# Kernel tuning notes

Measured on AMD Instinct MI355X. Metric: run time of the kernel, lower is better.

Reference implementation:

```python
import jax, jax.numpy as jnp
import numpy as np

N_NODES = 50000
N_EDGES = 800000
IN_CH = 128
HID = 128
N_GRAPHS = 512


def setup_inputs() -> dict:
    key = jax.random.key(0)
    ks = jax.random.split(key, 12)
    x = jax.random.normal(ks[0], (N_NODES, IN_CH), dtype=jnp.float32)
    edge_index = jax.random.randint(ks[1], (2, N_EDGES), 0, N_NODES, dtype=jnp.int64)
    batch = jnp.sort(jax.random.randint(ks[2], (N_NODES,), 0, N_GRAPHS, dtype=jnp.int64))
    s = 0.05
    params = {
        'W1l': jax.random.normal(ks[3], (HID, IN_CH), dtype=jnp.float32) * s,
        'W1r': jax.random.normal(ks[4], (HID, IN_CH), dtype=jnp.float32) * s,
        'b1': jax.random.normal(ks[5], (HID,), dtype=jnp.float32) * s,
        'W2l': jax.random.normal(ks[6], (HID, HID), dtype=jnp.float32) * s,
        'W2r': jax.random.normal(ks[7], (HID, HID), dtype=jnp.float32) * s,
        'b2': jax.random.normal(ks[8], (HID,), dtype=jnp.float32) * s,
        'W3l': jax.random.normal(ks[9], (HID, HID), dtype=jnp.float32) * s,
        'W3r': jax.random.normal(ks[10], (HID, HID), dtype=jnp.float32) * s,
        'b3': jax.random.normal(ks[11], (HID,), dtype=jnp.float32) * s,
    }
    return {'x': x, 'edge_index': edge_index, 'batch': batch, **params}


def reference(x, edge_index, batch, W1l, W1r, b1, W2l, W2r, b2, W3l, W3r, b3):
    src = edge_index[0]
    dst = edge_index[1]
    n = x.shape[0]
    # in-degree for mean aggregation (nodes with no in-edges get 0 aggregate)
    deg = jax.ops.segment_sum(jnp.ones((src.shape[0],), x.dtype), dst, num_segments=n)
    inv_deg = (1.0 / jnp.maximum(deg, 1.0))[:, None]  # [N,1]

    def sage(h, Wl, Wr, b):
        # gather neighbor feats, scatter-mean to targets, then linear + root term
        agg = jax.ops.segment_sum(h[src], dst, num_segments=n) * inv_deg  # [N,d]
        return agg @ Wl.T + h @ Wr.T + b

    h = jax.nn.relu(sage(x, W1l, W1r, b1))
    h = jax.nn.relu(sage(h, W2l, W2r, b2))
    h = jax.nn.relu(sage(h, W3l, W3r, b3))

    # global mean pool over graph ids
    counts = jax.ops.segment_sum(jnp.ones((n,), h.dtype), batch, num_segments=N_GRAPHS)
    pooled = jax.ops.segment_sum(h, batch, num_segments=N_GRAPHS)
    return pooled / jnp.maximum(counts, 1.0)[:, None]
```

## Files before the change

### kernel.cpp

```cpp
#include <hip/hip_runtime.h>

#define N_NODES 50000
#define NP 50048
#define N_EDGES 800000
#define N_GRAPHS 512
#define F 128
#define ELLW 64

#define FILL_BLOCKS 3125
#define CASTX_BLOCKS 3128
#define CASTW_BLOCKS 48

typedef __bf16 bf16x8 __attribute__((ext_vector_type(8)));
typedef float f32x4 __attribute__((ext_vector_type(4)));
typedef unsigned short ushort_t;
typedef unsigned int uint_t;

__device__ inline ushort_t f2bf(float f) {
    uint_t u = __float_as_uint(f);
    u += 0x7FFFu + ((u >> 16) & 1u);
    return (ushort_t)(u >> 16);
}
__device__ inline float bf2f(ushort_t u) {
    return __uint_as_float(((uint_t)u) << 16);
}
__device__ inline uint_t pack2(float a, float b) {
    return (uint_t)f2bf(a) | ((uint_t)f2bf(b) << 16);
}

__global__ __launch_bounds__(256) void k_build(
    const float* __restrict__ x,
    const float* __restrict__ w0, const float* __restrict__ w1,
    const float* __restrict__ w2, const float* __restrict__ w3,
    const float* __restrict__ w4, const float* __restrict__ w5,
    const int* __restrict__ src, const int* __restrict__ dst,
    ushort_t* __restrict__ X, ushort_t* __restrict__ WB,
    int* __restrict__ cnt, ushort_t* __restrict__ ell) {
    int b = blockIdx.x;
    int t = threadIdx.x;
    if (b < FILL_BLOCKS) {
        int e = b * 256 + t;
        int d = dst[e];
        int pos = atomicAdd(&cnt[d], 1);
        if (pos < ELLW) ell[(d << 6) + pos] = (ushort_t)src[e];
    } else if (b < FILL_BLOCKS + CASTX_BLOCKS) {
        int i = ((b - FILL_BLOCKS) * 256 + t) * 8;
        uint4 o = make_uint4(0, 0, 0, 0);
        if (i < N_NODES * F) {
            float4 v0 = *(const float4*)&x[i];
            float4 v1 = *(const float4*)&x[i + 4];
            o = make_uint4(pack2(v0.x, v0.y), pack2(v0.z, v0.w),
                           pack2(v1.x, v1.y), pack2(v1.z, v1.w));
        }
        *(uint4*)&X[i] = o;
    } else {
        int idx = (b - FILL_BLOCKS - CASTX_BLOCKS) * 256 + t;
        int m = idx >> 11;
        int o = (idx & 2047) * 8;
        const float* s = w0;
        if (m == 1) s = w1; else if (m == 2) s = w2; else if (m == 3) s = w3;
        else if (m == 4) s = w4; else if (m == 5) s = w5;
        float4 v0 = *(const float4*)&s[o];
        float4 v1 = *(const float4*)&s[o + 4];
        *(uint4*)&WB[m * 16384 + o] =
            make_uint4(pack2(v0.x, v0.y), pack2(v0.z, v0.w),
                       pack2(v1.x, v1.y), pack2(v1.z, v1.w));
    }
}

__device__ inline void addrow(float* a, uint4 v) {
    a[0] += __uint_as_float(v.x << 16); a[1] += __uint_as_float(v.x & 0xFFFF0000u);
    a[2] += __uint_as_float(v.y << 16); a[3] += __uint_as_float(v.y & 0xFFFF0000u);
    a[4] += __uint_as_float(v.z << 16); a[5] += __uint_as_float(v.z & 0xFFFF0000u);
    a[6] += __uint_as_float(v.w << 16); a[7] += __uint_as_float(v.w & 0xFFFF0000u);
}

__global__ __launch_bounds__(256) void k_gather(const ushort_t* __restrict__ h,
                                                const ushort_t* __restrict__ ell,
                                                const int* __restrict__ cnt,
                                                ushort_t* __restrict__ agg) {
    int t = blockIdx.x * 256 + threadIdx.x;
    int n = t >> 4;
    int lane = t & 15;
    if (n >= N_NODES) return;
    int deg = min(cnt[n], ELLW);
    const ushort_t* el = ell + (n << 6);
    const uint4* h4 = (const uint4*)h;
    float ax[8], ay[8];
#pragma unroll
    for (int j = 0; j < 8; j++) { ax[j] = 0.f; ay[j] = 0.f; }
    int i = 0;
    for (; i + 8 <= deg; i += 8) {
        uint4 iv = *(const uint4*)&el[i];
        int s0 = iv.x & 0xFFFF, s1 = iv.x >> 16;
        int s2 = iv.y & 0xFFFF, s3 = iv.y >> 16;
        int s4 = iv.z & 0xFFFF, s5 = iv.z >> 16;
        int s6 = iv.w & 0xFFFF, s7 = iv.w >> 16;
        uint4 v0 = h4[(size_t)s0 * 16 + lane];
        uint4 v1 = h4[(size_t)s1 * 16 + lane];
        uint4 v2 = h4[(size_t)s2 * 16 + lane];
        uint4 v3 = h4[(size_t)s3 * 16 + lane];
        uint4 v4 = h4[(size_t)s4 * 16 + lane];
        uint4 v5 = h4[(size_t)s5 * 16 + lane];
        uint4 v6 = h4[(size_t)s6 * 16 + lane];
        uint4 v7 = h4[(size_t)s7 * 16 + lane];
        addrow(ax, v0); addrow(ay, v1); addrow(ax, v2); addrow(ay, v3);
        addrow(ax, v4); addrow(ay, v5); addrow(ax, v6); addrow(ay, v7);
    }
    for (; i < deg; i++) {
        uint4 v0 = h4[(size_t)el[i] * 16 + lane];
        addrow(ax, v0);
    }
    float sc = 1.0f / fmaxf((float)deg, 1.0f);
    uint_t r[4];
#pragma unroll
    for (int j = 0; j < 4; j++)
        r[j] = pack2((ax[2 * j] + ay[2 * j]) * sc,
                     (ax[2 * j + 1] + ay[2 * j + 1]) * sc);
    ((uint4*)agg)[(size_t)n * 16 + lane] = make_uint4(r[0], r[1], r[2], r[3]);
}

__global__ __launch_bounds__(256) void k_linear(const ushort_t* __restrict__ agg,
                                                const ushort_t* h,
                                                const ushort_t* __restrict__ Wl,
                                                const ushort_t* __restrict__ Wr,
                                                const float* __restrict__ bias,
                                                ushort_t* out) {
    __shared__ uint4 Alds4[512];
    __shared__ uint4 Blds4[1024];
    ushort_t* Alds = (ushort_t*)Alds4;
    ushort_t* Blds = (ushort_t*)Blds4;

    int t = threadIdx.x;
    int w = t >> 6;
    int lane = t & 63;
    int bm = blockIdx.x * 64;
    int wm = (w & 1) * 32;
    int wn = (w >> 1) * 64;
    int lrow = lane & 15;
    int kg = lane >> 4;

    f32x4 acc[2][4];
#pragma unroll
    for (int i = 0; i < 2; i++)
#pragma unroll
        for (int j = 0; j < 4; j++) acc[i][j] = (f32x4){0.f, 0.f, 0.f, 0.f};

    for (int iter = 0; iter < 4; iter++) {
        int kk = iter * 64;
        const ushort_t* A = (kk < 128) ? agg : h;
        const ushort_t* W = (kk < 128) ? Wl : Wr;
        int k0 = kk & 127;

        __syncthreads();
#pragma unroll
        for (int p = 0; p < 2; p++) {
            int chunkA = p * 4 + w;
            const ushort_t* gA = A + (size_t)(bm + lane) * F + k0 + chunkA * 8;
            ushort_t* lA = Alds + (size_t)(chunkA * 64) * 8;
            __builtin_amdgcn_global_load_lds(
                (const __attribute__((address_space(1))) void*)gA,
                (__attribute__((address_space(3))) void*)lA, 16, 0, 0);
        }
#pragma unroll
        for (int p = 0; p < 4; p++) {
            int chunkB = p * 2 + (w >> 1);
            int rbase = (w & 1) * 64;
            const ushort_t* gB = W + (size_t)(rbase + lane) * F + k0 + chunkB * 8;
            ushort_t* lB = Blds + (size_t)(chunkB * 128 + rbase) * 8;
            __builtin_amdgcn_global_load_lds(
                (const __attribute__((address_space(1))) void*)gB,
                (__attribute__((address_space(3))) void*)lB, 16, 0, 0);
        }
        __syncthreads();

#pragma unroll
        for (int ks = 0; ks < 2; ks++) {
            bf16x8 af[2], bfr[4];
#pragma unroll
            for (int i = 0; i < 2; i++)
                af[i] = *(const bf16x8*)(Alds +
                    (size_t)((ks * 4 + kg) * 64 + wm + i * 16 + lrow) * 8);
#pragma unroll
            for (int j = 0; j < 4; j++)
                bfr[j] = *(const bf16x8*)(Blds +
                    (size_t)((ks * 4 + kg) * 128 + wn + j * 16 + lrow) * 8);
#pragma unroll
            for (int i = 0; i < 2; i++)
#pragma unroll
                for (int j = 0; j < 4; j++)
                    acc[i][j] = __builtin_amdgcn_mfma_f32_16x16x32_bf16(
                        af[i], bfr[j], acc[i][j], 0, 0, 0);
        }
    }

    int quad = lane >> 4;
#pragma unroll
    for (int j = 0; j < 4; j++) {
        int c = wn + j * 16 + lrow;
        float bj = bias[c];
#pragma unroll
        for (int i = 0; i < 2; i++) {
#pragma unroll
            for (int r = 0; r < 4; r++) {
                int row = bm + wm + i * 16 + quad * 4 + r;
                if (row < N_NODES) {
                    float v = fmaxf(acc[i][j][r] + bj, 0.0f);
                    out[(size_t)row * F + c] = f2bf(v);
                }
            }
        }
    }
}

__global__ __launch_bounds__(128) void k_pool(const ushort_t* __restrict__ h,
                                              const int* __restrict__ batch,
                                              float* __restrict__ out) {
    int g = blockIdx.x;
    int j = threadIdx.x;
    int lo = 0, hi = N_NODES;
    while (lo < hi) {
        int m = (lo + hi) >> 1;
        if (batch[m] < g) lo = m + 1; else hi = m;
    }
    int start = lo;
    lo = start; hi = N_NODES;
    while (lo < hi) {
        int m = (lo + hi) >> 1;
        if (batch[m] < g + 1) lo = m + 1; else hi = m;
    }
    int end = lo;
    float s = 0.0f;
    for (int n = start; n < end; n++) s += bf2f(h[(size_t)n * F + j]);
    out[g * F + j] = s / fmaxf((float)(end - start), 1.0f);
}

extern "C" void kernel_launch(void* const* d_in, const int* in_sizes, int n_in,
                              void* d_out, int out_size, void* d_ws, size_t ws_size,
                              hipStream_t stream) {
    const float* x   = (const float*)d_in[0];
    const int*   ei  = (const int*)d_in[1];
    const int* batch = (const int*)d_in[2];
    const float* W1l = (const float*)d_in[3];
    const float* W1r = (const float*)d_in[4];
    const float* b1  = (const float*)d_in[5];
    const float* W2l = (const float*)d_in[6];
    const float* W2r = (const float*)d_in[7];
    const float* b2  = (const float*)d_in[8];
    const float* W3l = (const float*)d_in[9];
    const float* W3r = (const float*)d_in[10];
    const float* b3  = (const float*)d_in[11];
    float* out = (float*)d_out;

    const int* src = ei;
    const int* dst = ei + N_EDGES;

    ushort_t* X   = (ushort_t*)d_ws;
    ushort_t* H   = X + (size_t)NP * F;
    ushort_t* AGG = H + (size_t)NP * F;
    ushort_t* WB  = AGG + (size_t)NP * F;
    int* cnt = (int*)(WB + 6 * 16384);
    ushort_t* ell = (ushort_t*)(cnt + 50176);

    const ushort_t* Wb1l = WB;
    const ushort_t* Wb1r = WB + 16384;
    const ushort_t* Wb2l = WB + 2 * 16384;
    const ushort_t* Wb2r = WB + 3 * 16384;
    const ushort_t* Wb3l = WB + 4 * 16384;
    const ushort_t* Wb3r = WB + 5 * 16384;

    hipMemsetAsync(cnt, 0, 50176 * sizeof(int), stream);
    k_build<<<FILL_BLOCKS + CASTX_BLOCKS + CASTW_BLOCKS, 256, 0, stream>>>(
        x, W1l, W1r, W2l, W2r, W3l, W3r, src, dst, X, WB, cnt, ell);

    const int gatherBlocks = (N_NODES * 16 + 255) / 256;
    const int linearBlocks = NP / 64;

    k_gather<<<gatherBlocks, 256, 0, stream>>>(X, ell, cnt, AGG);
    k_linear<<<linearBlocks, 256, 0, stream>>>(AGG, X, Wb1l, Wb1r, b1, H);
    k_gather<<<gatherBlocks, 256, 0, stream>>>(H, ell, cnt, AGG);
    k_linear<<<linearBlocks, 256, 0, stream>>>(AGG, H, Wb2l, Wb2r, b2, H);
    k_gather<<<gatherBlocks, 256, 0, stream>>>(H, ell, cnt, AGG);
    k_linear<<<linearBlocks, 256, 0, stream>>>(AGG, H, Wb3l, Wb3r, b3, H);

    k_pool<<<N_GRAPHS, 128, 0, stream>>>(H, batch, out);
}
```

Measured before the change: 336.0 us.

## Fuse neighbor gather into linear kernel, keep aggregate in LDS

```diff
diff --git a/kernel.cpp b/kernel.cpp
--- a/kernel.cpp
+++ b/kernel.cpp
@@ -75,70 +75,60 @@
     a[6] += __uint_as_float(v.w << 16); a[7] += __uint_as_float(v.w & 0xFFFF0000u);
 }
 
-__global__ __launch_bounds__(256) void k_gather(const ushort_t* __restrict__ h,
-                                                const ushort_t* __restrict__ ell,
-                                                const int* __restrict__ cnt,
-                                                ushort_t* __restrict__ agg) {
-    int t = blockIdx.x * 256 + threadIdx.x;
-    int n = t >> 4;
-    int lane = t & 15;
-    if (n >= N_NODES) return;
-    int deg = min(cnt[n], ELLW);
-    const ushort_t* el = ell + (n << 6);
-    const uint4* h4 = (const uint4*)h;
-    float ax[8], ay[8];
-#pragma unroll
-    for (int j = 0; j < 8; j++) { ax[j] = 0.f; ay[j] = 0.f; }
-    int i = 0;
-    for (; i + 8 <= deg; i += 8) {
-        uint4 iv = *(const uint4*)&el[i];
-        int s0 = iv.x & 0xFFFF, s1 = iv.x >> 16;
-        int s2 = iv.y & 0xFFFF, s3 = iv.y >> 16;
-        int s4 = iv.z & 0xFFFF, s5 = iv.z >> 16;
-        int s6 = iv.w & 0xFFFF, s7 = iv.w >> 16;
-        uint4 v0 = h4[(size_t)s0 * 16 + lane];
-        uint4 v1 = h4[(size_t)s1 * 16 + lane];
-        uint4 v2 = h4[(size_t)s2 * 16 + lane];
-        uint4 v3 = h4[(size_t)s3 * 16 + lane];
-        uint4 v4 = h4[(size_t)s4 * 16 + lane];
-        uint4 v5 = h4[(size_t)s5 * 16 + lane];
-        uint4 v6 = h4[(size_t)s6 * 16 + lane];
-        uint4 v7 = h4[(size_t)s7 * 16 + lane];
-        addrow(ax, v0); addrow(ay, v1); addrow(ax, v2); addrow(ay, v3);
-        addrow(ax, v4); addrow(ay, v5); addrow(ax, v6); addrow(ay, v7);
-    }
-    for (; i < deg; i++) {
-        uint4 v0 = h4[(size_t)el[i] * 16 + lane];
-        addrow(ax, v0);
-    }
-    float sc = 1.0f / fmaxf((float)deg, 1.0f);
-    uint_t r[4];
-#pragma unroll
-    for (int j = 0; j < 4; j++)
-        r[j] = pack2((ax[2 * j] + ay[2 * j]) * sc,
-                     (ax[2 * j + 1] + ay[2 * j + 1]) * sc);
-    ((uint4*)agg)[(size_t)n * 16 + lane] = make_uint4(r[0], r[1], r[2], r[3]);
-}
-
-__global__ __launch_bounds__(256) void k_linear(const ushort_t* __restrict__ agg,
-                                                const ushort_t* h,
-                                                const ushort_t* __restrict__ Wl,
-                                                const ushort_t* __restrict__ Wr,
-                                                const float* __restrict__ bias,
-                                                ushort_t* out) {
-    __shared__ uint4 Alds4[512];
+__global__ __launch_bounds__(256) void k_layer(
+    const ushort_t* __restrict__ hin,
+    const ushort_t* __restrict__ ell, const int* __restrict__ cnt,
+    const ushort_t* __restrict__ Wl, const ushort_t* __restrict__ Wr,
+    const float* __restrict__ bias, ushort_t* __restrict__ hout) {
+    __shared__ uint4 Agg4[64 * 17];
+    __shared__ uint4 Hlds4[512];
     __shared__ uint4 Blds4[1024];
-    ushort_t* Alds = (ushort_t*)Alds4;
+    ushort_t* aggl = (ushort_t*)Agg4;
+    ushort_t* Hlds = (ushort_t*)Hlds4;
     ushort_t* Blds = (ushort_t*)Blds4;
 
     int t = threadIdx.x;
     int w = t >> 6;
     int lane = t & 63;
     int bm = blockIdx.x * 64;
+
+    int lane16 = t & 15;
+    int nslot = t >> 4;
+    const uint4* h4 = (const uint4*)hin;
+#pragma unroll
+    for (int round = 0; round < 4; round++) {
+        int ln = round * 16 + nslot;
+        int n = bm + ln;
+        int deg = min(cnt[n], ELLW);
+        const ushort_t* el = ell + ((size_t)n << 6);
+        float ax[8], ay[8];
+#pragma unroll
+        for (int j = 0; j < 8; j++) { ax[j] = 0.f; ay[j] = 0.f; }
+        int i = 0;
+        for (; i + 4 <= deg; i += 4) {
+            int s0 = el[i], s1 = el[i + 1], s2 = el[i + 2], s3 = el[i + 3];
+            uint4 v0 = h4[(size_t)s0 * 16 + lane16];
+            uint4 v1 = h4[(size_t)s1 * 16 + lane16];
+            uint4 v2 = h4[(size_t)s2 * 16 + lane16];
+            uint4 v3 = h4[(size_t)s3 * 16 + lane16];
+            addrow(ax, v0); addrow(ay, v1); addrow(ax, v2); addrow(ay, v3);
+        }
+        for (; i < deg; i++) {
+            uint4 v0 = h4[(size_t)el[i] * 16 + lane16];
+            addrow(ax, v0);
+        }
+        float sc = 1.0f / fmaxf((float)deg, 1.0f);
+        Agg4[ln * 17 + lane16] = make_uint4(
+            pack2((ax[0] + ay[0]) * sc, (ax[1] + ay[1]) * sc),
+            pack2((ax[2] + ay[2]) * sc, (ax[3] + ay[3]) * sc),
+            pack2((ax[4] + ay[4]) * sc, (ax[5] + ay[5]) * sc),
+            pack2((ax[6] + ay[6]) * sc, (ax[7] + ay[7]) * sc));
+    }
+
     int wm = (w & 1) * 32;
     int wn = (w >> 1) * 64;
     int lrow = lane & 15;
-    int kg = lane >> 4;
+    int kg = (lane >> 4) & 3;
 
     f32x4 acc[2][4];
 #pragma unroll
@@ -146,21 +136,22 @@
 #pragma unroll
         for (int j = 0; j < 4; j++) acc[i][j] = (f32x4){0.f, 0.f, 0.f, 0.f};
 
+#pragma unroll
     for (int iter = 0; iter < 4; iter++) {
-        int kk = iter * 64;
-        const ushort_t* A = (kk < 128) ? agg : h;
-        const ushort_t* W = (kk < 128) ? Wl : Wr;
-        int k0 = kk & 127;
+        const ushort_t* W = (iter < 2) ? Wl : Wr;
+        int k0 = (iter & 1) * 64;
 
         __syncthreads();
-#pragma unroll
-        for (int p = 0; p < 2; p++) {
-            int chunkA = p * 4 + w;
-            const ushort_t* gA = A + (size_t)(bm + lane) * F + k0 + chunkA * 8;
-            ushort_t* lA = Alds + (size_t)(chunkA * 64) * 8;
-            __builtin_amdgcn_global_load_lds(
-                (const __attribute__((address_space(1))) void*)gA,
-                (__attribute__((address_space(3))) void*)lA, 16, 0, 0);
+        if (iter >= 2) {
+#pragma unroll
+            for (int p = 0; p < 2; p++) {
+                int chunkA = p * 4 + w;
+                const ushort_t* gA = hin + (size_t)(bm + lane) * F + k0 + chunkA * 8;
+                ushort_t* lA = Hlds + (size_t)(chunkA * 64) * 8;
+                __builtin_amdgcn_global_load_lds(
+                    (const __attribute__((address_space(1))) void*)gA,
+                    (__attribute__((address_space(3))) void*)lA, 16, 0, 0);
+            }
         }
 #pragma unroll
         for (int p = 0; p < 4; p++) {
@@ -178,9 +169,15 @@
         for (int ks = 0; ks < 2; ks++) {
             bf16x8 af[2], bfr[4];
 #pragma unroll
-            for (int i = 0; i < 2; i++)
-                af[i] = *(const bf16x8*)(Alds +
-                    (size_t)((ks * 4 + kg) * 64 + wm + i * 16 + lrow) * 8);
+            for (int i = 0; i < 2; i++) {
+                int row = wm + i * 16 + lrow;
+                if (iter < 2)
+                    af[i] = *(const bf16x8*)(aggl +
+                        (size_t)(row * 17 + iter * 8 + ks * 4 + kg) * 8);
+                else
+                    af[i] = *(const bf16x8*)(Hlds +
+                        (size_t)((ks * 4 + kg) * 64 + row) * 8);
+            }
 #pragma unroll
             for (int j = 0; j < 4; j++)
                 bfr[j] = *(const bf16x8*)(Blds +
@@ -206,7 +203,7 @@
                 int row = bm + wm + i * 16 + quad * 4 + r;
                 if (row < N_NODES) {
                     float v = fmaxf(acc[i][j][r] + bj, 0.0f);
-                    out[(size_t)row * F + c] = f2bf(v);
+                    hout[(size_t)row * F + c] = f2bf(v);
                 }
             }
         }
@@ -256,9 +253,9 @@
     const int* dst = ei + N_EDGES;
 
     ushort_t* X   = (ushort_t*)d_ws;
-    ushort_t* H   = X + (size_t)NP * F;
-    ushort_t* AGG = H + (size_t)NP * F;
-    ushort_t* WB  = AGG + (size_t)NP * F;
+    ushort_t* HA  = X + (size_t)NP * F;
+    ushort_t* HB  = HA + (size_t)NP * F;
+    ushort_t* WB  = HB + (size_t)NP * F;
     int* cnt = (int*)(WB + 6 * 16384);
     ushort_t* ell = (ushort_t*)(cnt + 50176);
 
@@ -273,15 +270,11 @@
     k_build<<<FILL_BLOCKS + CASTX_BLOCKS + CASTW_BLOCKS, 256, 0, stream>>>(
         x, W1l, W1r, W2l, W2r, W3l, W3r, src, dst, X, WB, cnt, ell);
 
-    const int gatherBlocks = (N_NODES * 16 + 255) / 256;
-    const int linearBlocks = NP / 64;
-
-    k_gather<<<gatherBlocks, 256, 0, stream>>>(X, ell, cnt, AGG);
-    k_linear<<<linearBlocks, 256, 0, stream>>>(AGG, X, Wb1l, Wb1r, b1, H);
-    k_gather<<<gatherBlocks, 256, 0, stream>>>(H, ell, cnt, AGG);
-    k_linear<<<linearBlocks, 256, 0, stream>>>(AGG, H, Wb2l, Wb2r, b2, H);
-    k_gather<<<gatherBlocks, 256, 0, stream>>>(H, ell, cnt, AGG);
-    k_linear<<<linearBlocks, 256, 0, stream>>>(AGG, H, Wb3l, Wb3r, b3, H);
-
-    k_pool<<<N_GRAPHS, 128, 0, stream>>>(H, batch, out);
-}
+    const int layerBlocks = NP / 64;
+
+    k_layer<<<layerBlocks, 256, 0, stream>>>(X, ell, cnt, Wb1l, Wb1r, b1, HA);
+    k_layer<<<layerBlocks, 256, 0, stream>>>(HA, ell, cnt, Wb2l, Wb2r, b2, HB);
+    k_layer<<<layerBlocks, 256, 0, stream>>>(HB, ell, cnt, Wb3l, Wb3r, b3, HA);
+
+    k_pool<<<N_GRAPHS, 128, 0, stream>>>(HA, batch, out);
+}
```

New measurement: 382.8 us. 1.14x slower.
